# Kernel tuning notes

Hardware: AMD Instinct MI355X
Metric: run time of the kernel (lower is better)

The kernel has to match this reference:

```python
import jax, jax.numpy as jnp
import numpy as np

DECAY = 0.99
EPS = 1e-05


def setup_inputs() -> dict:
    key = jax.random.key(0)
    k1, k2, k3 = jax.random.split(key, 3)
    B, H, W, D, K = 16, 32, 32, 256, 8192
    x = jax.random.normal(k1, (B, H, W, D), dtype=jnp.float32)
    embed = jax.random.normal(k2, (D, K), dtype=jnp.float32)
    cluster_size = jnp.zeros((K,), dtype=jnp.float32)
    embed_avg = jax.random.normal(k3, (D, K), dtype=jnp.float32)
    return {"x": x, "embed": embed, "cluster_size": cluster_size, "embed_avg": embed_avg}


def reference(x, embed, cluster_size, embed_avg):
    D, K = embed.shape
    flat = x.reshape(-1, D)  # (N, D)
    # squared L2 distances: ||f||^2 - 2 f.e + ||e||^2  -> (N, K)
    dist = (flat * flat).sum(1, keepdims=True) - 2.0 * (flat @ embed) + (embed * embed).sum(0, keepdims=True)
    idx = jnp.argmin(dist, axis=1)  # (N,)
    quantize = jnp.take(embed.T, idx, axis=0).reshape(x.shape)  # (B,H,W,D)
    # EMA codebook statistics (training branch)
    onehot_sum = jnp.zeros((K,), dtype=flat.dtype).at[idx].add(1.0)  # (K,)
    embed_sum = jax.ops.segment_sum(flat, idx, num_segments=K).T  # (D, K)
    new_cluster_size = cluster_size * DECAY + (1.0 - DECAY) * onehot_sum
    new_embed_avg = embed_avg * DECAY + (1.0 - DECAY) * embed_sum
    n = new_cluster_size.sum()
    cs = (new_cluster_size + EPS) / (n + K * EPS) * n
    new_embed = new_embed_avg / cs[None, :]
    latent_loss = jnp.mean((jax.lax.stop_gradient(quantize) - x) ** 2)
    quantize_st = x + jax.lax.stop_gradient(quantize - x)  # straight-through
    return quantize_st, latent_loss, new_embed, new_cluster_size, new_embed_avg
```

## Files before the change

kernel.cpp:

```cpp
#include <hip/hip_runtime.h>

constexpr int NROWS = 16384;
constexpr int D     = 256;
constexpr int K     = 8192;

constexpr float DECAY = 0.99f;
constexpr float OMD   = 0.01f;
constexpr float EPSF  = 1e-5f;

constexpr size_t OUT_Q    = 0;
constexpr size_t OUT_LOSS = (size_t)NROWS * D;
constexpr size_t OUT_NE   = OUT_LOSS + 1;
constexpr size_t OUT_NCS  = OUT_NE + (size_t)D * K;
constexpr size_t OUT_NEA  = OUT_NCS + K;

constexpr size_t WS_KEYS  = 0;
constexpr size_t WS_ENORM = WS_KEYS + (size_t)NROWS * 8;
constexpr size_t WS_XH    = ((WS_ENORM + (size_t)K * 4 + 4095) / 4096) * 4096;
constexpr size_t WS_XL    = WS_XH + (size_t)NROWS * D * 2;
constexpr size_t WS_EHT   = WS_XL + (size_t)NROWS * D * 2;
constexpr size_t WS_ELT   = WS_EHT + (size_t)K * D * 2;

typedef unsigned int u32;
typedef unsigned short u16;
typedef unsigned long long u64;
typedef __attribute__((ext_vector_type(8))) short bf16x8;
typedef __attribute__((ext_vector_type(4))) float f32x4;
typedef __attribute__((ext_vector_type(4))) u32 u32x4;
typedef __attribute__((ext_vector_type(2))) u32 u32x2;

__device__ __forceinline__ u16 f2bf(float f) {
    u32 u = __float_as_uint(f);
    u32 r = (u + 0x7FFFu + ((u >> 16) & 1u)) >> 16;
    return (u16)r;
}
__device__ __forceinline__ float bf2f(u16 h) {
    return __uint_as_float((u32)h << 16);
}

__device__ __forceinline__ void gl_lds16(const void* g, void* l) {
    __builtin_amdgcn_global_load_lds(
        (const __attribute__((address_space(1))) u32*)g,
        (__attribute__((address_space(3))) u32*)l, 16, 0, 0);
}

__global__ void pre_kernel(const float* __restrict__ x,
                           const float* __restrict__ embed,
                           const float* __restrict__ cluster_size,
                           u16* __restrict__ xh, u16* __restrict__ xl,
                           u16* __restrict__ ehT, u16* __restrict__ elT,
                           float* __restrict__ enorm,
                           u64* __restrict__ keys,
                           float* __restrict__ ncs_out,
                           float* __restrict__ loss_out) {
    const int bid = blockIdx.x;
    const int t   = threadIdx.x;

    if (bid >= 176) {
        size_t g = (size_t)(bid - 176) * 256 + t;
        float4 v = *(const float4*)&x[g * 4];
        u16 h0 = f2bf(v.x), h1 = f2bf(v.y), h2 = f2bf(v.z), h3 = f2bf(v.w);
        u16 l0 = f2bf(v.x - bf2f(h0)), l1 = f2bf(v.y - bf2f(h1));
        u16 l2 = f2bf(v.z - bf2f(h2)), l3 = f2bf(v.w - bf2f(h3));
        u32x2 hp, lp;
        hp.x = (u32)h0 | ((u32)h1 << 16); hp.y = (u32)h2 | ((u32)h3 << 16);
        lp.x = (u32)l0 | ((u32)l1 << 16); lp.y = (u32)l2 | ((u32)l3 << 16);
        ((u32x2*)xh)[g] = hp;
        ((u32x2*)xl)[g] = lp;
        return;
    }
    if (bid >= 144) {
        int i = (bid - 144) * 256 + t;
        ncs_out[i] = DECAY * cluster_size[i];
        return;
    }
    if (bid >= 128) {
        int idx = (bid - 128) * 256 + t;
        #pragma unroll
        for (int j = 0; j < 4; ++j) keys[j * 4096 + idx] = ~0ull;
        if (bid == 128 && t == 0) loss_out[0] = 0.f;
        return;
    }

    __shared__ float tile[64][68];
    const int kBase = bid * 64;
    const int dl = t >> 2;
    const int kl = t >> 2;
    const int qq = t & 3;
    float nacc = 0.f;

    for (int dBase = 0; dBase < D; dBase += 64) {
        #pragma unroll
        for (int i = 0; i < 4; ++i) {
            int kk = qq * 16 + i * 4;
            float4 v = *(const float4*)&embed[(size_t)(dBase + dl) * K + kBase + kk];
            tile[dl][kk + 0] = v.x; tile[dl][kk + 1] = v.y;
            tile[dl][kk + 2] = v.z; tile[dl][kk + 3] = v.w;
        }
        __syncthreads();
        u32 hp[8], lp[8];
        float s = 0.f;
        #pragma unroll
        for (int j = 0; j < 16; ++j) {
            float f = tile[qq * 16 + j][kl];
            s = fmaf(f, f, s);
            u16 hb = f2bf(f);
            u16 lb = f2bf(f - bf2f(hb));
            if (j & 1) { hp[j >> 1] |= (u32)hb << 16; lp[j >> 1] |= (u32)lb << 16; }
            else       { hp[j >> 1]  = hb;            lp[j >> 1]  = lb; }
        }
        s += __shfl_down(s, 1);
        s += __shfl_down(s, 2);
        if (qq == 0) nacc += s;

        size_t o = ((size_t)(kBase + kl) * D + dBase + qq * 16) >> 1;
        u32x4 a, b;
        a.x = hp[0]; a.y = hp[1]; a.z = hp[2]; a.w = hp[3];
        b.x = hp[4]; b.y = hp[5]; b.z = hp[6]; b.w = hp[7];
        *(u32x4*)&((u32*)ehT)[o]     = a;
        *(u32x4*)&((u32*)ehT)[o + 4] = b;
        a.x = lp[0]; a.y = lp[1]; a.z = lp[2]; a.w = lp[3];
        b.x = lp[4]; b.y = lp[5]; b.z = lp[6]; b.w = lp[7];
        *(u32x4*)&((u32*)elT)[o]     = a;
        *(u32x4*)&((u32*)elT)[o + 4] = b;
        __syncthreads();
    }
    if (qq == 0) enorm[kBase + kl] = nacc;
}

__global__ __launch_bounds__(512, 2) void dist_argmin_mfma(
        const u16* __restrict__ xh, const u16* __restrict__ xl,
        const u16* __restrict__ ehT, const u16* __restrict__ elT,
        const float* __restrict__ enorm,
        u64* __restrict__ keys) {
    __shared__ u16 lds[2][32768];

    const int tid  = threadIdx.x;
    const int lane = tid & 63;
    const int wave = tid >> 6;
    const int wm   = wave >> 1;
    const int wn   = wave & 1;
    const int r = lane & 15, g = lane >> 4;
    const int rowBase = blockIdx.y * 256;
    const int colBase = blockIdx.x * 256;

    f32x4 acc[4][8];
    #pragma unroll
    for (int i = 0; i < 4; ++i)
        #pragma unroll
        for (int j = 0; j < 8; ++j) acc[i][j] = (f32x4)0.f;

    const int chunk8 = (((tid & 3) ^ ((tid >> 3) & 3)) * 8);
    const int arow   = tid >> 2;
    const size_t a0 = (size_t)(rowBase + arow) * D + chunk8;
    const size_t a1 = (size_t)(rowBase + 128 + arow) * D + chunk8;
    const int bmat   = tid >> 8;
    const int qrow   = (tid & 255) >> 2;
    const int bcol0  = (qrow < 32) ? qrow : (96 + qrow);
    const size_t bq0 = (size_t)(colBase + bcol0) * D + chunk8;
    const u16* bsrc  = bmat ? elT : ehT;

    const int kx = (g ^ ((r >> 1) & 3)) * 8;

    #define ST_XH0(buf, ks) gl_lds16(&xh[a0 + (ks) * 32], &lds[buf][tid * 8])
    #define ST_XH1(buf, ks) gl_lds16(&xh[a1 + (ks) * 32], &lds[buf][4096 + tid * 8])
    #define ST_XL0(buf, ks) gl_lds16(&xl[a0 + (ks) * 32], &lds[buf][8192 + tid * 8])
    #define ST_XL1(buf, ks) gl_lds16(&xl[a1 + (ks) * 32], &lds[buf][12288 + tid * 8])
    #define ST_B(buf, ks, q) \
        gl_lds16(&bsrc[bq0 + (size_t)(q) * 32 * D + (ks) * 32], \
                 &lds[buf][16384 + (q) * 4096 + tid * 8])

    ST_B(0, 0, 0); ST_XH0(0, 0); ST_B(0, 0, 1); ST_XH1(0, 0);
    ST_B(0, 0, 2); ST_XL0(0, 0); ST_B(0, 0, 3); ST_XL1(0, 0);
    ST_B(1, 1, 0); ST_XH0(1, 1); ST_B(1, 1, 1); ST_XH1(1, 1);
    ST_B(1, 1, 2); ST_XL0(1, 1);

    bf16x8 fah[4], fal[4], fbh[2], fbl[2];

    #define MFMA3(i, j, jj)                                                          \
        acc[i][j] = __builtin_amdgcn_mfma_f32_16x16x32_bf16(fah[i], fbh[jj], acc[i][j], 0, 0, 0); \
        acc[i][j] = __builtin_amdgcn_mfma_f32_16x16x32_bf16(fah[i], fbl[jj], acc[i][j], 0, 0, 0); \
        acc[i][j] = __builtin_amdgcn_mfma_f32_16x16x32_bf16(fal[i], fbh[jj], acc[i][j], 0, 0, 0)

    #pragma unroll
    for (int ks = 0; ks < 8; ++ks) {
        const int c = ks & 1;
        const u16* L = lds[c];

        if (ks == 7) asm volatile("s_waitcnt vmcnt(0)" ::: "memory");
        else         asm volatile("s_waitcnt vmcnt(6)" ::: "memory");
        __builtin_amdgcn_s_barrier();
        __builtin_amdgcn_sched_barrier(0);

        #pragma unroll
        for (int i = 0; i < 4; ++i) {
            fah[i] = *(const bf16x8*)&L[((wm * 64 + i * 16 + r) * 32) + kx];
            fal[i] = *(const bf16x8*)&L[8192 + ((wm * 64 + i * 16 + r) * 32) + kx];
        }
        #pragma unroll
        for (int jj = 0; jj < 2; ++jj) {
            const int qr = wn * 32 + jj * 16 + r;
            fbh[jj] = *(const bf16x8*)&L[16384 + qr * 32 + kx];
            fbl[jj] = *(const bf16x8*)&L[16384 + 2048 + qr * 32 + kx];
        }
        if (ks <= 6) { ST_B(c ^ 1, ks + 1, 3); ST_XL1(c ^ 1, ks + 1); }
        asm volatile("s_waitcnt lgkmcnt(0)" ::: "memory");
        __builtin_amdgcn_sched_barrier(0);
        __builtin_amdgcn_s_setprio(1);
        #pragma unroll
        for (int i = 0; i < 4; ++i) { MFMA3(i, 0, 0); MFMA3(i, 1, 1); }
        __builtin_amdgcn_s_setprio(0);
        __builtin_amdgcn_s_barrier();
        __builtin_amdgcn_sched_barrier(0);

        #pragma unroll
        for (int p = 1; p < 4; ++p) {
            #pragma unroll
            for (int jj = 0; jj < 2; ++jj) {
                const int qr = wn * 32 + jj * 16 + r;
                fbh[jj] = *(const bf16x8*)&L[16384 + p * 4096 + qr * 32 + kx];
                fbl[jj] = *(const bf16x8*)&L[16384 + p * 4096 + 2048 + qr * 32 + kx];
            }
            if (ks <= 5) {
                ST_B(c, ks + 2, p - 1);
                if      (p == 1) ST_XH0(c, ks + 2);
                else if (p == 2) ST_XH1(c, ks + 2);
                else             ST_XL0(c, ks + 2);
            }
            asm volatile("s_waitcnt lgkmcnt(0)" ::: "memory");
            __builtin_amdgcn_sched_barrier(0);
            __builtin_amdgcn_s_setprio(1);
            #pragma unroll
            for (int i = 0; i < 4; ++i) { MFMA3(i, 2 * p, 0); MFMA3(i, 2 * p + 1, 1); }
            __builtin_amdgcn_s_setprio(0);
            __builtin_amdgcn_s_barrier();
            __builtin_amdgcn_sched_barrier(0);
        }
    }
    #undef MFMA3
    #undef ST_XH0
    #undef ST_XH1
    #undef ST_XL0
    #undef ST_XL1
    #undef ST_B

    float en[8];
    #pragma unroll
    for (int j = 0; j < 8; ++j) en[j] = enorm[colBase + wn * 128 + j * 16 + r];

    #pragma unroll
    for (int i = 0; i < 4; ++i) {
        #pragma unroll
        for (int p4 = 0; p4 < 4; ++p4) {
            float best = __builtin_inff();
            int bk = 0;
            #pragma unroll
            for (int j = 0; j < 8; ++j) {
                float s = fmaf(-2.f, acc[i][j][p4], en[j]);
                int ccol = colBase + wn * 128 + j * 16 + r;
                if (s < best) { best = s; bk = ccol; }
            }
            u32 u = __float_as_uint(best);
            u ^= (u >> 31) ? 0xFFFFFFFFu : 0x80000000u;
            u64 key = ((u64)u << 32) | (u32)bk;
            #pragma unroll
            for (int m = 1; m < 16; m <<= 1) {
                u64 o = __shfl_xor(key, m);
                key = o < key ? o : key;
            }
            if (r == 0)
                atomicMin(&keys[rowBase + wm * 64 + i * 16 + g * 4 + p4], key);
        }
    }
}

__global__ void postprocess_kernel(const float* __restrict__ x,
                                   const u16* __restrict__ ehT,
                                   const u16* __restrict__ elT,
                                   const u64* __restrict__ keys,
                                   float* __restrict__ q_out,
                                   float* __restrict__ loss_out,
                                   float* __restrict__ acc_t,
                                   float* __restrict__ ncs_out) {
    const int w    = threadIdx.x >> 6;
    const int lane = threadIdx.x & 63;
    const int r    = blockIdx.x * 4 + w;
    const u32 k = (u32)keys[r];

    float4 xv = *(const float4*)&x[(size_t)r * D + lane * 4];
    size_t uo = ((size_t)k * D >> 1) + lane * 2;
    u32x2 hp = *(const u32x2*)&((const u32*)ehT)[uo];
    u32x2 lp = *(const u32x2*)&((const u32*)elT)[uo];
    float q0 = __uint_as_float(hp.x << 16)         + __uint_as_float(lp.x << 16);
    float q1 = __uint_as_float(hp.x & 0xFFFF0000u) + __uint_as_float(lp.x & 0xFFFF0000u);
    float q2 = __uint_as_float(hp.y << 16)         + __uint_as_float(lp.y << 16);
    float q3 = __uint_as_float(hp.y & 0xFFFF0000u) + __uint_as_float(lp.y & 0xFFFF0000u);
    *(float4*)&q_out[(size_t)r * D + lane * 4] = make_float4(q0, q1, q2, q3);

    float* dst = &acc_t[(size_t)k * D + lane * 4];
    atomicAdd(dst + 0, xv.x);
    atomicAdd(dst + 1, xv.y);
    atomicAdd(dst + 2, xv.z);
    atomicAdd(dst + 3, xv.w);
    if (lane == 0) atomicAdd(&ncs_out[k], OMD);

    float d0 = q0 - xv.x, d1 = q1 - xv.y, d2 = q2 - xv.z, d3 = q3 - xv.w;
    float lsum = fmaf(d0, d0, fmaf(d1, d1, fmaf(d2, d2, d3 * d3)));
    #pragma unroll
    for (int off = 32; off > 0; off >>= 1) lsum += __shfl_down(lsum, off);
    __shared__ float wsum[4];
    if (lane == 0) wsum[w] = lsum;
    __syncthreads();
    if (threadIdx.x == 0) {
        float s = wsum[0] + wsum[1] + wsum[2] + wsum[3];
        atomicAdd(loss_out, s * (1.0f / ((float)NROWS * (float)D)));
    }
}

__global__ void ema_finalize_kernel(const float* __restrict__ embed_avg,
                                    const float* __restrict__ acc_t,
                                    const float* __restrict__ ncs_out,
                                    const float* __restrict__ cluster_size,
                                    float* __restrict__ nea_out,
                                    float* __restrict__ ne_out) {
    __shared__ float tile[64][68];
    __shared__ float wsums[4];
    const int kBase = blockIdx.x * 64;
    const int dBase = blockIdx.y * 64;
    const int t = threadIdx.x;

    float cs_part = 0.f;
    #pragma unroll
    for (int j = 0; j < K / 256; ++j) cs_part += cluster_size[j * 256 + t];
    #pragma unroll
    for (int off = 32; off > 0; off >>= 1) cs_part += __shfl_down(cs_part, off);
    if ((t & 63) == 0) wsums[t >> 6] = cs_part;

    {
        const int kl = t >> 2, q = t & 3;
        #pragma unroll
        for (int i = 0; i < 4; ++i) {
            int dd = q * 16 + i * 4;
            float4 v = *(const float4*)&acc_t[(size_t)(kBase + kl) * D + dBase + dd];
            tile[kl][dd + 0] = v.x; tile[kl][dd + 1] = v.y;
            tile[kl][dd + 2] = v.z; tile[kl][dd + 3] = v.w;
        }
    }
    __syncthreads();
    const float cssum = wsums[0] + wsums[1] + wsums[2] + wsums[3];
    const float n = DECAY * cssum + OMD * (float)NROWS;
    const float inv_na = 1.0f / (n + (float)K * EPSF);
    const int dl = t >> 2, q = t & 3;
    #pragma unroll
    for (int i = 0; i < 4; ++i) {
        int kk = q * 16 + i * 4;
        size_t o = (size_t)(dBase + dl) * K + kBase + kk;
        float4 ea = *(const float4*)&embed_avg[o];
        float4 nea, ne;
        #pragma unroll
        for (int c = 0; c < 4; ++c) {
            float v  = DECAY * ((const float*)&ea)[c] + OMD * tile[kk + c][dl];
            float cs = (ncs_out[kBase + kk + c] + EPSF) * inv_na * n;
            ((float*)&nea)[c] = v;
            ((float*)&ne)[c]  = v / cs;
        }
        *(float4*)&nea_out[o] = nea;
        *(float4*)&ne_out[o]  = ne;
    }
}

extern "C" void kernel_launch(void* const* d_in, const int* in_sizes, int n_in,
                              void* d_out, int out_size, void* d_ws, size_t ws_size,
                              hipStream_t stream) {
    (void)in_sizes; (void)n_in; (void)out_size; (void)ws_size;
    const float* x            = (const float*)d_in[0];
    const float* embed        = (const float*)d_in[1];
    const float* cluster_size = (const float*)d_in[2];
    const float* embed_avg    = (const float*)d_in[3];
    float* out = (float*)d_out;

    char* ws = (char*)d_ws;
    u64*   keys  = (u64*)(ws + WS_KEYS);
    float* enorm = (float*)(ws + WS_ENORM);
    u16*   xh    = (u16*)(ws + WS_XH);
    u16*   xl    = (u16*)(ws + WS_XL);
    u16*   ehT   = (u16*)(ws + WS_EHT);
    u16*   elT   = (u16*)(ws + WS_ELT);
    float* acc_t = (float*)(ws + WS_XH);

    float* q_out    = out + OUT_Q;
    float* loss_out = out + OUT_LOSS;
    float* ne_out   = out + OUT_NE;
    float* ncs_out  = out + OUT_NCS;
    float* nea_out  = out + OUT_NEA;

    pre_kernel<<<dim3(176 + NROWS * D / 4 / 256), dim3(256), 0, stream>>>(
        x, embed, cluster_size, xh, xl, ehT, elT, enorm, keys, ncs_out, loss_out);

    dist_argmin_mfma<<<dim3(K / 256, NROWS / 256), dim3(512), 0, stream>>>(
        xh, xl, ehT, elT, enorm, keys);

    hipMemsetAsync(acc_t, 0, (size_t)K * D * 4, stream);
    postprocess_kernel<<<dim3(NROWS / 4), dim3(256), 0, stream>>>(
        x, ehT, elT, keys, q_out, loss_out, acc_t, ncs_out);
    ema_finalize_kernel<<<dim3(K / 64, D / 64), dim3(256), 0, stream>>>(
        embed_avg, acc_t, ncs_out, cluster_size, nea_out, ne_out);
}
```

Before: 317.0 us.

## Switch distance GEMM to 32x32x16 MFMA with double-buffered B fragments

Replaces the 16x16x32 bf16 MFMA tiling with 32x32x16 instructions, reorganising accumulators into 2x4 f32x16 tiles and rewriting the LDS fragment reads to match. B fragments are ping-ponged between two register sets so the next phase's LDS reads overlap the current MFMAs, waiting with lgkmcnt(4) instead of draining everything. The aim is fewer fragment loads per flop and better LDS/MFMA overlap. It also changes the argmin epilogue to a 32-lane shuffle reduction with a new row mapping, which could be wrong if the index math is off, and the larger accumulators raise register pressure.

```diff
diff --git a/kernel.cpp b/kernel.cpp
--- a/kernel.cpp
+++ b/kernel.cpp
@@ -25,7 +25,7 @@
 typedef unsigned short u16;
 typedef unsigned long long u64;
 typedef __attribute__((ext_vector_type(8))) short bf16x8;
-typedef __attribute__((ext_vector_type(4))) float f32x4;
+typedef __attribute__((ext_vector_type(16))) float f32x16;
 typedef __attribute__((ext_vector_type(4))) u32 u32x4;
 typedef __attribute__((ext_vector_type(2))) u32 u32x2;
 
@@ -140,15 +140,16 @@
     const int wave = tid >> 6;
     const int wm   = wave >> 1;
     const int wn   = wave & 1;
-    const int r = lane & 15, g = lane >> 4;
+    const int c5   = lane & 31;
+    const int hi   = lane >> 5;
     const int rowBase = blockIdx.y * 256;
     const int colBase = blockIdx.x * 256;
 
-    f32x4 acc[4][8];
-    #pragma unroll
-    for (int i = 0; i < 4; ++i)
-        #pragma unroll
-        for (int j = 0; j < 8; ++j) acc[i][j] = (f32x4)0.f;
+    f32x16 acc[2][4];
+    #pragma unroll
+    for (int i = 0; i < 2; ++i)
+        #pragma unroll
+        for (int j = 0; j < 4; ++j) acc[i][j] = (f32x16)0.f;
 
     const int chunk8 = (((tid & 3) ^ ((tid >> 3) & 3)) * 8);
     const int arow   = tid >> 2;
@@ -160,8 +161,6 @@
     const size_t bq0 = (size_t)(colBase + bcol0) * D + chunk8;
     const u16* bsrc  = bmat ? elT : ehT;
 
-    const int kx = (g ^ ((r >> 1) & 3)) * 8;
-
     #define ST_XH0(buf, ks) gl_lds16(&xh[a0 + (ks) * 32], &lds[buf][tid * 8])
     #define ST_XH1(buf, ks) gl_lds16(&xh[a1 + (ks) * 32], &lds[buf][4096 + tid * 8])
     #define ST_XL0(buf, ks) gl_lds16(&xl[a0 + (ks) * 32], &lds[buf][8192 + tid * 8])
@@ -175,12 +174,40 @@
     ST_B(1, 1, 0); ST_XH0(1, 1); ST_B(1, 1, 1); ST_XH1(1, 1);
     ST_B(1, 1, 2); ST_XL0(1, 1);
 
-    bf16x8 fah[4], fal[4], fbh[2], fbl[2];
-
-    #define MFMA3(i, j, jj)                                                          \
-        acc[i][j] = __builtin_amdgcn_mfma_f32_16x16x32_bf16(fah[i], fbh[jj], acc[i][j], 0, 0, 0); \
-        acc[i][j] = __builtin_amdgcn_mfma_f32_16x16x32_bf16(fah[i], fbl[jj], acc[i][j], 0, 0, 0); \
-        acc[i][j] = __builtin_amdgcn_mfma_f32_16x16x32_bf16(fal[i], fbh[jj], acc[i][j], 0, 0, 0)
+    bf16x8 fah[2][2], fal[2][2];
+    bf16x8 fbhA[2], fblA[2], fbhB[2], fblB[2];
+
+    #define RD_A(Lp)                                                             \
+        do { _Pragma("unroll") for (int i_ = 0; i_ < 2; ++i_) {                  \
+            _Pragma("unroll") for (int s_ = 0; s_ < 2; ++s_) {                   \
+                const int row_ = wm * 64 + i_ * 32 + c5;                         \
+                const int ck_  = ((s_ * 2 + hi) ^ ((row_ >> 1) & 3)) * 8;        \
+                fah[i_][s_] = *(const bf16x8*)&(Lp)[row_ * 32 + ck_];            \
+                fal[i_][s_] = *(const bf16x8*)&(Lp)[8192 + row_ * 32 + ck_];     \
+        } } } while (0)
+
+    #define RD_B(Lp, p, FH, FL)                                                  \
+        do { _Pragma("unroll") for (int s_ = 0; s_ < 2; ++s_) {                   \
+            const int br_ = wn * 32 + c5;                                         \
+            const int ck_ = ((s_ * 2 + hi) ^ ((br_ >> 1) & 3)) * 8;               \
+            (FH)[s_] = *(const bf16x8*)&(Lp)[16384 + (p) * 4096 + br_ * 32 + ck_];        \
+            (FL)[s_] = *(const bf16x8*)&(Lp)[16384 + (p) * 4096 + 2048 + br_ * 32 + ck_]; \
+        } } while (0)
+
+    #define MFMA_PH(p, FH, FL)                                                    \
+        do { _Pragma("unroll") for (int s_ = 0; s_ < 2; ++s_) {                   \
+            acc[0][p] = __builtin_amdgcn_mfma_f32_32x32x16_bf16(fah[0][s_], (FH)[s_], acc[0][p], 0, 0, 0); \
+            acc[1][p] = __builtin_amdgcn_mfma_f32_32x32x16_bf16(fah[1][s_], (FH)[s_], acc[1][p], 0, 0, 0); \
+            acc[0][p] = __builtin_amdgcn_mfma_f32_32x32x16_bf16(fah[0][s_], (FL)[s_], acc[0][p], 0, 0, 0); \
+            acc[1][p] = __builtin_amdgcn_mfma_f32_32x32x16_bf16(fah[1][s_], (FL)[s_], acc[1][p], 0, 0, 0); \
+            acc[0][p] = __builtin_amdgcn_mfma_f32_32x32x16_bf16(fal[0][s_], (FH)[s_], acc[0][p], 0, 0, 0); \
+            acc[1][p] = __builtin_amdgcn_mfma_f32_32x32x16_bf16(fal[1][s_], (FH)[s_], acc[1][p], 0, 0, 0); \
+        } } while (0)
+
+    #define LGKM4() asm volatile("s_waitcnt lgkmcnt(4)" ::: "memory"); \
+                    __builtin_amdgcn_sched_barrier(0)
+    #define LGKM0() asm volatile("s_waitcnt lgkmcnt(0)" ::: "memory"); \
+                    __builtin_amdgcn_sched_barrier(0)
 
     #pragma unroll
     for (int ks = 0; ks < 8; ++ks) {
@@ -192,84 +219,81 @@
         __builtin_amdgcn_s_barrier();
         __builtin_amdgcn_sched_barrier(0);
 
-        #pragma unroll
-        for (int i = 0; i < 4; ++i) {
-            fah[i] = *(const bf16x8*)&L[((wm * 64 + i * 16 + r) * 32) + kx];
-            fal[i] = *(const bf16x8*)&L[8192 + ((wm * 64 + i * 16 + r) * 32) + kx];
-        }
-        #pragma unroll
-        for (int jj = 0; jj < 2; ++jj) {
-            const int qr = wn * 32 + jj * 16 + r;
-            fbh[jj] = *(const bf16x8*)&L[16384 + qr * 32 + kx];
-            fbl[jj] = *(const bf16x8*)&L[16384 + 2048 + qr * 32 + kx];
-        }
+        RD_A(L);
+        RD_B(L, 0, fbhA, fblA);
+        RD_B(L, 1, fbhB, fblB);
         if (ks <= 6) { ST_B(c ^ 1, ks + 1, 3); ST_XL1(c ^ 1, ks + 1); }
-        asm volatile("s_waitcnt lgkmcnt(0)" ::: "memory");
-        __builtin_amdgcn_sched_barrier(0);
+        LGKM4();
         __builtin_amdgcn_s_setprio(1);
-        #pragma unroll
-        for (int i = 0; i < 4; ++i) { MFMA3(i, 0, 0); MFMA3(i, 1, 1); }
+        MFMA_PH(0, fbhA, fblA);
         __builtin_amdgcn_s_setprio(0);
         __builtin_amdgcn_s_barrier();
         __builtin_amdgcn_sched_barrier(0);
 
-        #pragma unroll
-        for (int p = 1; p < 4; ++p) {
-            #pragma unroll
-            for (int jj = 0; jj < 2; ++jj) {
-                const int qr = wn * 32 + jj * 16 + r;
-                fbh[jj] = *(const bf16x8*)&L[16384 + p * 4096 + qr * 32 + kx];
-                fbl[jj] = *(const bf16x8*)&L[16384 + p * 4096 + 2048 + qr * 32 + kx];
-            }
-            if (ks <= 5) {
-                ST_B(c, ks + 2, p - 1);
-                if      (p == 1) ST_XH0(c, ks + 2);
-                else if (p == 2) ST_XH1(c, ks + 2);
-                else             ST_XL0(c, ks + 2);
-            }
-            asm volatile("s_waitcnt lgkmcnt(0)" ::: "memory");
-            __builtin_amdgcn_sched_barrier(0);
-            __builtin_amdgcn_s_setprio(1);
-            #pragma unroll
-            for (int i = 0; i < 4; ++i) { MFMA3(i, 2 * p, 0); MFMA3(i, 2 * p + 1, 1); }
-            __builtin_amdgcn_s_setprio(0);
-            __builtin_amdgcn_s_barrier();
-            __builtin_amdgcn_sched_barrier(0);
-        }
-    }
-    #undef MFMA3
+        RD_B(L, 2, fbhA, fblA);
+        if (ks <= 5) { ST_B(c, ks + 2, 0); ST_XH0(c, ks + 2); }
+        LGKM4();
+        __builtin_amdgcn_s_setprio(1);
+        MFMA_PH(1, fbhB, fblB);
+        __builtin_amdgcn_s_setprio(0);
+        __builtin_amdgcn_s_barrier();
+        __builtin_amdgcn_sched_barrier(0);
+
+        RD_B(L, 3, fbhB, fblB);
+        if (ks <= 5) { ST_B(c, ks + 2, 1); ST_XH1(c, ks + 2); }
+        LGKM4();
+        __builtin_amdgcn_s_setprio(1);
+        MFMA_PH(2, fbhA, fblA);
+        __builtin_amdgcn_s_setprio(0);
+        __builtin_amdgcn_s_barrier();
+        __builtin_amdgcn_sched_barrier(0);
+
+        if (ks <= 5) { ST_B(c, ks + 2, 2); ST_XL0(c, ks + 2); }
+        LGKM0();
+        __builtin_amdgcn_s_setprio(1);
+        MFMA_PH(3, fbhB, fblB);
+        __builtin_amdgcn_s_setprio(0);
+        __builtin_amdgcn_s_barrier();
+        __builtin_amdgcn_sched_barrier(0);
+    }
+    #undef MFMA_PH
+    #undef RD_A
+    #undef RD_B
+    #undef LGKM4
+    #undef LGKM0
     #undef ST_XH0
     #undef ST_XH1
     #undef ST_XL0
     #undef ST_XL1
     #undef ST_B
 
-    float en[8];
-    #pragma unroll
-    for (int j = 0; j < 8; ++j) en[j] = enorm[colBase + wn * 128 + j * 16 + r];
-
-    #pragma unroll
-    for (int i = 0; i < 4; ++i) {
-        #pragma unroll
-        for (int p4 = 0; p4 < 4; ++p4) {
+    float en[4];
+    #pragma unroll
+    for (int j = 0; j < 4; ++j) en[j] = enorm[colBase + wn * 128 + j * 32 + c5];
+
+    #pragma unroll
+    for (int i = 0; i < 2; ++i) {
+        #pragma unroll
+        for (int p = 0; p < 16; ++p) {
             float best = __builtin_inff();
             int bk = 0;
             #pragma unroll
-            for (int j = 0; j < 8; ++j) {
-                float s = fmaf(-2.f, acc[i][j][p4], en[j]);
-                int ccol = colBase + wn * 128 + j * 16 + r;
+            for (int j = 0; j < 4; ++j) {
+                float s = fmaf(-2.f, acc[i][j][p], en[j]);
+                int ccol = colBase + wn * 128 + j * 32 + c5;
                 if (s < best) { best = s; bk = ccol; }
             }
             u32 u = __float_as_uint(best);
             u ^= (u >> 31) ? 0xFFFFFFFFu : 0x80000000u;
             u64 key = ((u64)u << 32) | (u32)bk;
             #pragma unroll
-            for (int m = 1; m < 16; m <<= 1) {
+            for (int m = 1; m < 32; m <<= 1) {
                 u64 o = __shfl_xor(key, m);
                 key = o < key ? o : key;
             }
-            if (r == 0)
-                atomicMin(&keys[rowBase + wm * 64 + i * 16 + g * 4 + p4], key);
+            if (c5 == 0)
+                atomicMin(&keys[rowBase + wm * 64 + i * 32 +
+                                (p & 3) + 8 * (p >> 2) + 4 * hi], key);
         }
     }
 }
```

New measurement: 347.8 us. 1.1x slower.
